# Optimization experiments

Hardware: AMD Instinct MI355X
Metric: run time of the kernel (lower is better)

Reference implementation:

```python
import jax, jax.numpy as jnp
import numpy as np
import math

HEADS = 16
D_MODEL = 1024
HEAD_DIM = D_MODEL // HEADS
B, S = 2, 2048


def setup_inputs() -> dict:
    key = jax.random.key(0)
    ks = jax.random.split(key, 12)
    sc = 1.0 / math.sqrt(D_MODEL)
    inp = {
        "query": jax.random.normal(ks[0], (B, S, D_MODEL), jnp.float32),
        "key_t": jax.random.normal(ks[1], (B, S, D_MODEL), jnp.float32),
        "value": jax.random.normal(ks[2], (B, S, D_MODEL), jnp.float32),
        "mask": jax.random.randint(ks[3], (B, 1, 1, S), 0, 2, jnp.int32),
        "Wq": jax.random.normal(ks[4], (D_MODEL, D_MODEL), jnp.float32) * sc,
        "bq": jnp.zeros((D_MODEL,), jnp.float32),
        "Wk": jax.random.normal(ks[5], (D_MODEL, D_MODEL), jnp.float32) * sc,
        "bk": jnp.zeros((D_MODEL,), jnp.float32),
        "Wv": jax.random.normal(ks[6], (D_MODEL, D_MODEL), jnp.float32) * sc,
        "bv": jnp.zeros((D_MODEL,), jnp.float32),
        "Wo": jax.random.normal(ks[7], (D_MODEL, D_MODEL), jnp.float32) * sc,
        "bo": jnp.zeros((D_MODEL,), jnp.float32),
    }
    return inp


def _split_heads(x):
    # [B, S, D] -> [B, H, S, Dh]
    b, s, _ = x.shape
    return x.reshape(b, s, HEADS, HEAD_DIM).transpose(0, 2, 1, 3)


def reference(query, key_t, value, mask, Wq, bq, Wk, bk, Wv, bv, Wo, bo):
    # Linear projections (torch Linear: x @ W.T + b)
    q = _split_heads(query @ Wq.T + bq)
    k = _split_heads(key_t @ Wk.T + bk)
    v = _split_heads(value @ Wv.T + bv)
    # Scaled dot-product attention; scale by sqrt(head_dim) = query.size(-1) after split
    scores = jnp.einsum("bhqd,bhkd->bhqk", q, k) / math.sqrt(HEAD_DIM)
    scores = jnp.where(mask == 0, jnp.float32(-1e9), scores)
    prob = jax.nn.softmax(scores, axis=-1)
    # dropout is identity at inference
    attn = jnp.einsum("bhqk,bhkd->bhqd", prob, v)
    # [B, H, S, Dh] -> [B, S, D]
    attn = attn.transpose(0, 2, 1, 3).reshape(query.shape[0], -1, D_MODEL)
    return attn @ Wo.T + bo
```

## Files before the change

kernel.cpp:

```cpp
#include <hip/hip_runtime.h>
#include <hip/hip_bf16.h>

typedef __bf16 bf16;
typedef __bf16 bf16x8 __attribute__((ext_vector_type(8)));
typedef __bf16 bf16x4 __attribute__((ext_vector_type(4)));
typedef float  f32x4  __attribute__((ext_vector_type(4)));
typedef float  f32x16 __attribute__((ext_vector_type(16)));

#define AS1 __attribute__((address_space(1)))
#define AS3 __attribute__((address_space(3)))

__device__ __forceinline__ void gload_lds16(const bf16* g, bf16* l) {
    __builtin_amdgcn_global_load_lds((const AS1 unsigned int*)g,
                                     (AS3 unsigned int*)l, 16, 0, 0);
}

__global__ __launch_bounds__(256) void cast8_k(
    const float* __restrict__ s0, const float* __restrict__ s1,
    const float* __restrict__ s2, const float* __restrict__ s3,
    const float* __restrict__ s4, const float* __restrict__ s5,
    const float* __restrict__ s6,
    bf16* __restrict__ d0, bf16* __restrict__ d1, bf16* __restrict__ d2,
    bf16* __restrict__ d3, bf16* __restrict__ d4, bf16* __restrict__ d5,
    bf16* __restrict__ d6,
    const int* __restrict__ m, float* __restrict__ mb,
    int n_big, int n_small) {
    int z = blockIdx.z;
    int i = (blockIdx.x * 256 + threadIdx.x) * 8;
    if (z == 7) {
        if (i >= 4096) return;
        int4 a = *(const int4*)(m + i);
        int4 b = *(const int4*)(m + i + 4);
        float4 o0, o1;
        o0.x = (a.x == 0) ? -1.442695e9f : -17.3123405f;
        o0.y = (a.y == 0) ? -1.442695e9f : -17.3123405f;
        o0.z = (a.z == 0) ? -1.442695e9f : -17.3123405f;
        o0.w = (a.w == 0) ? -1.442695e9f : -17.3123405f;
        o1.x = (b.x == 0) ? -1.442695e9f : -17.3123405f;
        o1.y = (b.y == 0) ? -1.442695e9f : -17.3123405f;
        o1.z = (b.z == 0) ? -1.442695e9f : -17.3123405f;
        o1.w = (b.w == 0) ? -1.442695e9f : -17.3123405f;
        *(float4*)(mb + i) = o0;
        *(float4*)(mb + i + 4) = o1;
        return;
    }
    const float* s = (z == 0) ? s0 : (z == 1) ? s1 : (z == 2) ? s2
                   : (z == 3) ? s3 : (z == 4) ? s4 : (z == 5) ? s5 : s6;
    bf16* d = (z == 0) ? d0 : (z == 1) ? d1 : (z == 2) ? d2
            : (z == 3) ? d3 : (z == 4) ? d4 : (z == 5) ? d5 : d6;
    int n = (z < 3) ? n_big : n_small;
    if (i >= n) return;
    float4 a = *(const float4*)(s + i);
    float4 b = *(const float4*)(s + i + 4);
    bf16x8 o;
    o[0] = (bf16)a.x; o[1] = (bf16)a.y; o[2] = (bf16)a.z; o[3] = (bf16)a.w;
    o[4] = (bf16)b.x; o[5] = (bf16)b.y; o[6] = (bf16)b.z; o[7] = (bf16)b.w;
    *(bf16x8*)(d + i) = o;
}

template <typename OUT_T, bool TRANS>
__device__ __forceinline__ void gemm32_core(
    const bf16* __restrict__ A, const bf16* __restrict__ W,
    const float* __restrict__ bias, OUT_T* __restrict__ C,
    int M, int N, int K) {
    __shared__ bf16 Asm[128 * 64];
    __shared__ bf16 Bsm[128 * 64];
    const int lane = threadIdx.x & 63;
    const int w = threadIdx.x >> 6;
    const int l31 = lane & 31;
    const int h = lane >> 5;
    const int x7 = l31 & 7;
    const int m0 = blockIdx.x * 128;
    const int n0 = blockIdx.y * 128;
    const int srow = lane >> 3;
    const int scol = ((lane & 7) ^ srow) * 8;
    const int wm = (w & 1) * 64;
    const int wn = (w >> 1) * 64;

    f32x16 acc[2][2] = {};

    for (int k0 = 0; k0 < K; k0 += 64) {
#pragma unroll
        for (int c = 0; c < 4; ++c) {
            int r = w * 32 + c * 8;
            gload_lds16(A + (size_t)(m0 + r + srow) * K + k0 + scol, &Asm[r * 64]);
            gload_lds16(W + (size_t)(n0 + r + srow) * K + k0 + scol, &Bsm[r * 64]);
        }
        __syncthreads();
#pragma unroll
        for (int step = 0; step < 4; ++step) {
            bf16x8 af[2], bfv[2];
#pragma unroll
            for (int i = 0; i < 2; ++i)
                af[i] = *(const bf16x8*)&Asm[(wm + i * 32 + l31) * 64 +
                                             (((step * 2 + h) ^ x7) * 8)];
#pragma unroll
            for (int j = 0; j < 2; ++j)
                bfv[j] = *(const bf16x8*)&Bsm[(wn + j * 32 + l31) * 64 +
                                              (((step * 2 + h) ^ x7) * 8)];
#pragma unroll
            for (int i = 0; i < 2; ++i)
#pragma unroll
                for (int j = 0; j < 2; ++j)
                    acc[i][j] = TRANS
                        ? __builtin_amdgcn_mfma_f32_32x32x16_bf16(bfv[j], af[i],
                                                                  acc[i][j], 0, 0, 0)
                        : __builtin_amdgcn_mfma_f32_32x32x16_bf16(af[i], bfv[j],
                                                                  acc[i][j], 0, 0, 0);
        }
        __syncthreads();
    }
    if (!TRANS) {
#pragma unroll
        for (int i = 0; i < 2; ++i)
#pragma unroll
            for (int j = 0; j < 2; ++j) {
                int col = n0 + wn + j * 32 + l31;
                float bv = bias[col];
#pragma unroll
                for (int g = 0; g < 4; ++g)
#pragma unroll
                    for (int rr = 0; rr < 4; ++rr) {
                        int row = m0 + wm + i * 32 + rr + g * 8 + 4 * h;
                        C[(size_t)row * N + col] =
                            (OUT_T)(acc[i][j][g * 4 + rr] + bv);
                    }
            }
    } else {
#pragma unroll
        for (int i = 0; i < 2; ++i) {
            int s = m0 + wm + i * 32 + l31;
            int b = s >> 11;
            int sl = s & 2047;
            int sp = (sl & ~12) | ((sl & 4) << 1) | ((sl & 8) >> 1);
#pragma unroll
            for (int j = 0; j < 2; ++j)
#pragma unroll
                for (int g = 0; g < 4; ++g) {
                    float4 bv4 = *(const float4*)&bias[n0 + wn + j * 32 + g * 8 + 4 * h];
#pragma unroll
                    for (int rr = 0; rr < 4; ++rr) {
                        int n = n0 + wn + j * 32 + g * 8 + 4 * h + rr;
                        C[(size_t)(b * 1024 + n) * 2048 + sp] =
                            (OUT_T)(acc[i][j][g * 4 + rr] + (&bv4.x)[rr]);
                    }
                }
        }
    }
}

__global__ __launch_bounds__(256) void gemm_qkv(
    const bf16* __restrict__ qb, const bf16* __restrict__ kb, const bf16* __restrict__ vb,
    const bf16* __restrict__ Wq, const bf16* __restrict__ Wk, const bf16* __restrict__ Wv,
    const float* __restrict__ bq, const float* __restrict__ bk, const float* __restrict__ bv,
    bf16* __restrict__ Qp, bf16* __restrict__ Kp, bf16* __restrict__ VpT) {
    int z = blockIdx.z;
    if (z == 2) {
        gemm32_core<bf16, true>(vb, Wv, bv, VpT, 4096, 1024, 1024);
    } else {
        const bf16* A = (z == 0) ? qb : kb;
        const bf16* W = (z == 0) ? Wq : Wk;
        const float* bi = (z == 0) ? bq : bk;
        bf16* C = (z == 0) ? Qp : Kp;
        gemm32_core<bf16, false>(A, W, bi, C, 4096, 1024, 1024);
    }
}

__global__ __launch_bounds__(256) void gemm_out_fused(
    const bf16* __restrict__ Op, const float* __restrict__ Lp,
    const bf16* __restrict__ W, const float* __restrict__ bias,
    float* __restrict__ C) {
    __shared__ bf16 Asm[64 * 64];
    __shared__ bf16 Bsm[128 * 64];
    const int id = blockIdx.x;
    const int m0 = (id & 63) * 64;
    const int n0 = (id >> 6) * 128;
    const int lane = threadIdx.x & 63;
    const int w = threadIdx.x >> 6;
    const int l31 = lane & 31;
    const int h = lane >> 5;
    const int x7 = l31 & 7;
    const int srow = lane >> 3;
    const int l7 = lane & 7;
    const int scol = (l7 ^ srow) * 8;
    const int wm = (w & 1) * 32;
    const int wn = (w >> 1) * 64;

    f32x16 acc[2] = {};

    for (int k0 = 0; k0 < 1024; k0 += 64) {
#pragma unroll
        for (int c = 0; c < 2; ++c) {
            int r = w * 16 + c * 8;
            int row = m0 + r + srow;
            int colb = k0 + scol;
            int b = row >> 11, q = row & 2047;
            int hh = colb >> 6, d = colb & 63;
            size_t l0i = (size_t)(b * 16 + hh) * 2048 + q;
            bf16x8 v0 = *(const bf16x8*)&Op[l0i * 64 + d];
            bf16x8 v1 = *(const bf16x8*)&Op[(l0i + 32 * 2048) * 64 + d];
            float inv = 1.0f / (Lp[l0i] + Lp[l0i + 32 * 2048]);
            bf16x8 o;
#pragma unroll
            for (int i = 0; i < 8; ++i)
                o[i] = (bf16)(((float)v0[i] + (float)v1[i]) * inv);
            *(bf16x8*)&Asm[(r + srow) * 64 + l7 * 8] = o;
        }
#pragma unroll
        for (int c = 0; c < 4; ++c) {
            int r = w * 32 + c * 8;
            gload_lds16(W + (size_t)(n0 + r + srow) * 1024 + k0 + scol, &Bsm[r * 64]);
        }
        __syncthreads();
#pragma unroll
        for (int step = 0; step < 4; ++step) {
            bf16x8 af = *(const bf16x8*)&Asm[(wm + l31) * 64 +
                                             (((step * 2 + h) ^ x7) * 8)];
            bf16x8 bfv[2];
#pragma unroll
            for (int j = 0; j < 2; ++j)
                bfv[j] = *(const bf16x8*)&Bsm[(wn + j * 32 + l31) * 64 +
                                              (((step * 2 + h) ^ x7) * 8)];
#pragma unroll
            for (int j = 0; j < 2; ++j)
                acc[j] = __builtin_amdgcn_mfma_f32_32x32x16_bf16(af, bfv[j],
                                                                 acc[j], 0, 0, 0);
        }
        __syncthreads();
    }
#pragma unroll
    for (int j = 0; j < 2; ++j) {
        int col = n0 + wn + j * 32 + l31;
        float bv = bias[col];
#pragma unroll
        for (int g = 0; g < 4; ++g)
#pragma unroll
            for (int rr = 0; rr < 4; ++rr) {
                int row = m0 + wm + rr + g * 8 + 4 * h;
                C[(size_t)row * 1024 + col] = acc[j][g * 4 + rr] + bv;
            }
    }
}

__global__ __launch_bounds__(256, 2) void attn_k(
    const bf16* __restrict__ Qp, const bf16* __restrict__ Kp,
    const bf16* __restrict__ VpT, const float* __restrict__ mb,
    bf16* __restrict__ Opart, float* __restrict__ Lpart) {
    __shared__ bf16 KV[2][2][64 * 64];
    const int g = blockIdx.x;
    const int qb = g >> 6;
    const int bh = (g & 63) >> 1;
    const int sp = g & 1;
    const int b = bh >> 4, hh = bh & 15;
    const int lane = threadIdx.x & 63, w = threadIdx.x >> 6;
    const int l31 = lane & 31, h = lane >> 5;
    const int x7 = l31 & 7;
    const int srow = lane >> 3, scol = ((lane & 7) ^ srow) * 8;
    const float SC = 0.125f * 1.44269504f;
    const int q0 = qb * 256;
    const int k0 = sp * 1024;

    const bf16* Kg = Kp + (size_t)(b * 2048) * 1024 + hh * 64;
    const bf16* Vg = VpT + (size_t)bh * 64 * 2048;
    const float* mbb = mb + b * 2048;

    auto stage = [&](int buf, int kt) {
#pragma unroll
        for (int c = 0; c < 2; ++c) {
            int r = w * 16 + c * 8;
            gload_lds16(Kg + (size_t)(kt + r + srow) * 1024 + scol,
                        &KV[buf][0][r * 64]);
            gload_lds16(Vg + (size_t)(r + srow) * 2048 + kt + scol,
                        &KV[buf][1][r * 64]);
        }
    };
    stage(0, k0);

    bf16x8 qf[2][4];
#pragma unroll
    for (int qg = 0; qg < 2; ++qg) {
        const bf16* Qbase =
            Qp + (size_t)(b * 2048 + q0 + w * 64 + qg * 32 + l31) * 1024 + hh * 64;
#pragma unroll
        for (int step = 0; step < 4; ++step)
            qf[qg][step] = *(const bf16x8*)(Qbase + step * 16 + h * 8);
    }

    f32x16 o[2][2] = {};
    float lsum[2] = {0.0f, 0.0f};

    for (int it = 0; it < 16; ++it) {
        __syncthreads();
        if (it < 15) stage((it + 1) & 1, k0 + (it + 1) * 64);
        const bf16* Ks = KV[it & 1][0];
        const bf16* Vs = KV[it & 1][1];
        const int kt = k0 + it * 64;

        bf16x8 pa[2][4];
#pragma unroll
        for (int kg = 0; kg < 2; ++kg) {
            f32x16 z0 = {}, z1 = {};
#pragma unroll
            for (int step = 0; step < 4; ++step) {
                bf16x8 kf = *(const bf16x8*)&Ks[(kg * 32 + l31) * 64 +
                                                (((step * 2 + h) ^ x7) * 8)];
                z0 = __builtin_amdgcn_mfma_f32_32x32x16_bf16(kf, qf[0][step], z0, 0, 0, 0);
                z1 = __builtin_amdgcn_mfma_f32_32x32x16_bf16(kf, qf[1][step], z1, 0, 0, 0);
            }
#pragma unroll
            for (int g = 0; g < 4; ++g) {
                float4 bia = *(const float4*)&mbb[kt + kg * 32 + g * 8 + 4 * h];
#pragma unroll
                for (int qg = 0; qg < 2; ++qg) {
                    const f32x16& z = qg ? z1 : z0;
                    float p0 = __builtin_amdgcn_exp2f(fmaf(z[g * 4 + 0], SC, bia.x));
                    float p1 = __builtin_amdgcn_exp2f(fmaf(z[g * 4 + 1], SC, bia.y));
                    float p2 = __builtin_amdgcn_exp2f(fmaf(z[g * 4 + 2], SC, bia.z));
                    float p3 = __builtin_amdgcn_exp2f(fmaf(z[g * 4 + 3], SC, bia.w));
                    lsum[qg] += (p0 + p1) + (p2 + p3);
                    bf16x8& pf = pa[qg][kg * 2 + (g >> 1)];
                    int jb = (g & 1) * 4;
                    pf[jb + 0] = (bf16)p0;
                    pf[jb + 1] = (bf16)p1;
                    pf[jb + 2] = (bf16)p2;
                    pf[jb + 3] = (bf16)p3;
                }
            }
        }
#pragma unroll
        for (int t = 0; t < 2; ++t)
#pragma unroll
            for (int kk = 0; kk < 4; ++kk) {
                bf16x8 vf = *(const bf16x8*)&Vs[(t * 32 + l31) * 64 +
                                                (((kk * 2 + h) ^ x7) * 8)];
                o[0][t] = __builtin_amdgcn_mfma_f32_32x32x16_bf16(pa[0][kk], vf, o[0][t], 0, 0, 0);
                o[1][t] = __builtin_amdgcn_mfma_f32_32x32x16_bf16(pa[1][kk], vf, o[1][t], 0, 0, 0);
            }
    }

    const size_t pbase = (size_t)(sp * 32 + bh) * 2048;
#pragma unroll
    for (int qg = 0; qg < 2; ++qg) {
        float ls = lsum[qg] + __shfl_xor(lsum[qg], 32, 64);
        if (h == 0)
            Lpart[pbase + q0 + w * 64 + qg * 32 + l31] = ls;
#pragma unroll
        for (int t = 0; t < 2; ++t)
#pragma unroll
            for (int g = 0; g < 4; ++g)
#pragma unroll
                for (int rr = 0; rr < 4; ++rr) {
                    int q = q0 + w * 64 + qg * 32 + rr + g * 8 + 4 * h;
                    Opart[(pbase + q) * 64 + t * 32 + l31] =
                        (bf16)o[qg][t][g * 4 + rr];
                }
    }
}

extern "C" void kernel_launch(void* const* d_in, const int* in_sizes, int n_in,
                              void* d_out, int out_size, void* d_ws, size_t ws_size,
                              hipStream_t stream) {
    const float* q   = (const float*)d_in[0];
    const float* kt  = (const float*)d_in[1];
    const float* v   = (const float*)d_in[2];
    const int* mask  = (const int*)d_in[3];
    const float* Wq  = (const float*)d_in[4];
    const float* bq  = (const float*)d_in[5];
    const float* Wk  = (const float*)d_in[6];
    const float* bk  = (const float*)d_in[7];
    const float* Wv  = (const float*)d_in[8];
    const float* bv  = (const float*)d_in[9];
    const float* Wo  = (const float*)d_in[10];
    const float* bo  = (const float*)d_in[11];
    float* out = (float*)d_out;

    char* ws = (char*)d_ws;
    const size_t SZ_IN = 4096ull * 1024 * 2;
    const size_t SZ_W  = 1024ull * 1024 * 2;
    bf16* qb  = (bf16*)(ws + 0 * SZ_IN);
    bf16* kb  = (bf16*)(ws + 1 * SZ_IN);
    bf16* vb  = (bf16*)(ws + 2 * SZ_IN);
    bf16* Wqb = (bf16*)(ws + 3 * SZ_IN);
    bf16* Wkb = (bf16*)(ws + 3 * SZ_IN + 1 * SZ_W);
    bf16* Wvb = (bf16*)(ws + 3 * SZ_IN + 2 * SZ_W);
    bf16* Wob = (bf16*)(ws + 3 * SZ_IN + 3 * SZ_W);
    bf16* Qp  = (bf16*)(ws + 3 * SZ_IN + 4 * SZ_W);
    bf16* Kp  = (bf16*)(ws + 4 * SZ_IN + 4 * SZ_W);
    bf16* VpT = (bf16*)(ws + 5 * SZ_IN + 4 * SZ_W);
    float* mb = (float*)(ws + 6 * SZ_IN + 4 * SZ_W);
    char*  p0 = ws + 6 * SZ_IN + 4 * SZ_W + (1 << 20);
    bf16* Opart = (bf16*)p0;
    float* Lpart = (float*)(p0 + 2ull * 32 * 2048 * 64 * 2);

    const int NIN = 4096 * 1024, NW = 1024 * 1024;
    cast8_k<<<dim3(NIN / 2048, 1, 8), 256, 0, stream>>>(
        q, kt, v, Wq, Wk, Wv, Wo, qb, kb, vb, Wqb, Wkb, Wvb, Wob,
        mask, mb, NIN, NW);

    gemm_qkv<<<dim3(32, 8, 3), 256, 0, stream>>>(qb, kb, vb, Wqb, Wkb, Wvb,
                                                 bq, bk, bv, Qp, Kp, VpT);
    attn_k<<<dim3(512), 256, 0, stream>>>(Qp, Kp, VpT, mb, Opart, Lpart);
    gemm_out_fused<<<dim3(512), 256, 0, stream>>>(Opart, Lpart, Wob, bo, out);
}
```

Baseline: 221.2 us.

## Halve attention query tile per block, double grid, add MFMA priority hints

The attention kernel now gives each wave 32 query rows instead of 64, so a block covers 128 queries and the grid grows from 512 to 1024 blocks. Launch bounds rise to 4 blocks per CU, cutting register pressure so more waves can be resident and hide latency. s_setprio hints are added around the MFMA sections so that waves doing matrix work get issue priority over waves running the softmax math. In exchange, each K/V tile staged in LDS is reused by half as many queries, which doubles K/V loads overall.

New measurement: 227.8 us. +3.0%, slower.

```diff
diff --git a/kernel.cpp b/kernel.cpp
--- a/kernel.cpp
+++ b/kernel.cpp
@@ -242,14 +242,14 @@
     }
 }
 
-__global__ __launch_bounds__(256, 2) void attn_k(
+__global__ __launch_bounds__(256, 4) void attn_k(
     const bf16* __restrict__ Qp, const bf16* __restrict__ Kp,
     const bf16* __restrict__ VpT, const float* __restrict__ mb,
     bf16* __restrict__ Opart, float* __restrict__ Lpart) {
     __shared__ bf16 KV[2][2][64 * 64];
     const int g = blockIdx.x;
     const int qb = g >> 6;
-    const int bh = (g & 63) >> 1;
+    const int bh = (g >> 1) & 31;
     const int sp = g & 1;
     const int b = bh >> 4, hh = bh & 15;
     const int lane = threadIdx.x & 63, w = threadIdx.x >> 6;
@@ -257,7 +257,7 @@
     const int x7 = l31 & 7;
     const int srow = lane >> 3, scol = ((lane & 7) ^ srow) * 8;
     const float SC = 0.125f * 1.44269504f;
-    const int q0 = qb * 256;
+    const int q0 = qb * 128;
     const int k0 = sp * 1024;
 
     const bf16* Kg = Kp + (size_t)(b * 2048) * 1024 + hh * 64;
@@ -276,18 +276,17 @@
     };
     stage(0, k0);
 
-    bf16x8 qf[2][4];
-#pragma unroll
-    for (int qg = 0; qg < 2; ++qg) {
+    bf16x8 qf[4];
+    {
         const bf16* Qbase =
-            Qp + (size_t)(b * 2048 + q0 + w * 64 + qg * 32 + l31) * 1024 + hh * 64;
+            Qp + (size_t)(b * 2048 + q0 + w * 32 + l31) * 1024 + hh * 64;
 #pragma unroll
         for (int step = 0; step < 4; ++step)
-            qf[qg][step] = *(const bf16x8*)(Qbase + step * 16 + h * 8);
-    }
-
-    f32x16 o[2][2] = {};
-    float lsum[2] = {0.0f, 0.0f};
+            qf[step] = *(const bf16x8*)(Qbase + step * 16 + h * 8);
+    }
+
+    f32x16 o[2] = {};
+    float lsum = 0.0f;
 
     for (int it = 0; it < 16; ++it) {
         __syncthreads();
@@ -296,65 +295,62 @@
         const bf16* Vs = KV[it & 1][1];
         const int kt = k0 + it * 64;
 
-        bf16x8 pa[2][4];
+        bf16x8 pa[4];
 #pragma unroll
         for (int kg = 0; kg < 2; ++kg) {
-            f32x16 z0 = {}, z1 = {};
+            f32x16 z = {};
+            __builtin_amdgcn_s_setprio(1);
 #pragma unroll
             for (int step = 0; step < 4; ++step) {
                 bf16x8 kf = *(const bf16x8*)&Ks[(kg * 32 + l31) * 64 +
                                                 (((step * 2 + h) ^ x7) * 8)];
-                z0 = __builtin_amdgcn_mfma_f32_32x32x16_bf16(kf, qf[0][step], z0, 0, 0, 0);
-                z1 = __builtin_amdgcn_mfma_f32_32x32x16_bf16(kf, qf[1][step], z1, 0, 0, 0);
-            }
+                z = __builtin_amdgcn_mfma_f32_32x32x16_bf16(kf, qf[step], z, 0, 0, 0);
+            }
+            __builtin_amdgcn_s_setprio(0);
 #pragma unroll
             for (int g = 0; g < 4; ++g) {
                 float4 bia = *(const float4*)&mbb[kt + kg * 32 + g * 8 + 4 * h];
-#pragma unroll
-                for (int qg = 0; qg < 2; ++qg) {
-                    const f32x16& z = qg ? z1 : z0;
-                    float p0 = __builtin_amdgcn_exp2f(fmaf(z[g * 4 + 0], SC, bia.x));
-                    float p1 = __builtin_amdgcn_exp2f(fmaf(z[g * 4 + 1], SC, bia.y));
-                    float p2 = __builtin_amdgcn_exp2f(fmaf(z[g * 4 + 2], SC, bia.z));
-                    float p3 = __builtin_amdgcn_exp2f(fmaf(z[g * 4 + 3], SC, bia.w));
-                    lsum[qg] += (p0 + p1) + (p2 + p3);
-                    bf16x8& pf = pa[qg][kg * 2 + (g >> 1)];
-                    int jb = (g & 1) * 4;
-                    pf[jb + 0] = (bf16)p0;
-                    pf[jb + 1] = (bf16)p1;
-                    pf[jb + 2] = (bf16)p2;
-                    pf[jb + 3] = (bf16)p3;
-                }
-            }
-        }
+                float p0 = __builtin_amdgcn_exp2f(fmaf(z[g * 4 + 0], SC, bia.x));
+                float p1 = __builtin_amdgcn_exp2f(fmaf(z[g * 4 + 1], SC, bia.y));
+                float p2 = __builtin_amdgcn_exp2f(fmaf(z[g * 4 + 2], SC, bia.z));
+                float p3 = __builtin_amdgcn_exp2f(fmaf(z[g * 4 + 3], SC, bia.w));
+                lsum += (p0 + p1) + (p2 + p3);
+                bf16x8& pf = pa[kg * 2 + (g >> 1)];
+                int jb = (g & 1) * 4;
+                pf[jb + 0] = (bf16)p0;
+                pf[jb + 1] = (bf16)p1;
+                pf[jb + 2] = (bf16)p2;
+                pf[jb + 3] = (bf16)p3;
+            }
+        }
+        __builtin_amdgcn_s_setprio(1);
 #pragma unroll
         for (int t = 0; t < 2; ++t)
 #pragma unroll
             for (int kk = 0; kk < 4; ++kk) {
                 bf16x8 vf = *(const bf16x8*)&Vs[(t * 32 + l31) * 64 +
                                                 (((kk * 2 + h) ^ x7) * 8)];
-                o[0][t] = __builtin_amdgcn_mfma_f32_32x32x16_bf16(pa[0][kk], vf, o[0][t], 0, 0, 0);
-                o[1][t] = __builtin_amdgcn_mfma_f32_32x32x16_bf16(pa[1][kk], vf, o[1][t], 0, 0, 0);
-            }
+                o[t] = __builtin_amdgcn_mfma_f32_32x32x16_bf16(pa[kk], vf, o[t], 0, 0, 0);
+            }
+        __builtin_amdgcn_s_setprio(0);
     }
 
     const size_t pbase = (size_t)(sp * 32 + bh) * 2048;
-#pragma unroll
-    for (int qg = 0; qg < 2; ++qg) {
-        float ls = lsum[qg] + __shfl_xor(lsum[qg], 32, 64);
+    {
+        float ls = lsum + __shfl_xor(lsum, 32, 64);
         if (h == 0)
-            Lpart[pbase + q0 + w * 64 + qg * 32 + l31] = ls;
-#pragma unroll
-        for (int t = 0; t < 2; ++t)
-#pragma unroll
-            for (int g = 0; g < 4; ++g)
-#pragma unroll
-                for (int rr = 0; rr < 4; ++rr) {
-                    int q = q0 + w * 64 + qg * 32 + rr + g * 8 + 4 * h;
-                    Opart[(pbase + q) * 64 + t * 32 + l31] =
-                        (bf16)o[qg][t][g * 4 + rr];
-                }
-    }
+            Lpart[pbase + q0 + w * 32 + l31] = ls;
+    }
+#pragma unroll
+    for (int t = 0; t < 2; ++t)
+#pragma unroll
+        for (int g = 0; g < 4; ++g)
+#pragma unroll
+            for (int rr = 0; rr < 4; ++rr) {
+                int q = q0 + w * 32 + rr + g * 8 + 4 * h;
+                Opart[(pbase + q) * 64 + t * 32 + l31] =
+                    (bf16)o[t][g * 4 + rr];
+            }
 }
 
 extern "C" void kernel_launch(void* const* d_in, const int* in_sizes, int n_in,
@@ -399,6 +395,6 @@
 
     gemm_qkv<<<dim3(32, 8, 3), 256, 0, stream>>>(qb, kb, vb, Wqb, Wkb, Wvb,
                                                  bq, bk, bv, Qp, Kp, VpT);
-    attn_k<<<dim3(512), 256, 0, stream>>>(Qp, Kp, VpT, mb, Opart, Lpart);
+    attn_k<<<dim3(1024), 256, 0, stream>>>(Qp, Kp, VpT, mb, Opart, Lpart);
     gemm_out_fused<<<dim3(512), 256, 0, stream>>>(Opart, Lpart, Wob, bo, out);
 }
```

## Fuse fp32-to-bf16 casts into GEMM tile loads and raise MFMA wave priority

Applied to the files above, without the earlier changes.

Removes the separate cast kernel that converted inputs and weights to bf16. The GEMMs now load fp32 directly and convert while staging tiles into LDS, using register loads instead of direct global-to-LDS loads. This drops a full write and read of the bf16 copies, but each GEMM tile reads twice the bytes and loses the async LDS load path. The attention kernel also raises wave priority around its MFMA blocks.

After: 263.9 us. +19.3%, slower.

```diff
diff --git a/kernel.cpp b/kernel.cpp
--- a/kernel.cpp
+++ b/kernel.cpp
@@ -15,52 +15,38 @@
                                      (AS3 unsigned int*)l, 16, 0, 0);
 }
 
-__global__ __launch_bounds__(256) void cast8_k(
-    const float* __restrict__ s0, const float* __restrict__ s1,
-    const float* __restrict__ s2, const float* __restrict__ s3,
-    const float* __restrict__ s4, const float* __restrict__ s5,
-    const float* __restrict__ s6,
-    bf16* __restrict__ d0, bf16* __restrict__ d1, bf16* __restrict__ d2,
-    bf16* __restrict__ d3, bf16* __restrict__ d4, bf16* __restrict__ d5,
-    bf16* __restrict__ d6,
-    const int* __restrict__ m, float* __restrict__ mb,
-    int n_big, int n_small) {
-    int z = blockIdx.z;
+__global__ __launch_bounds__(256) void mask_k(
+    const int* __restrict__ m, float* __restrict__ mb) {
     int i = (blockIdx.x * 256 + threadIdx.x) * 8;
-    if (z == 7) {
-        if (i >= 4096) return;
-        int4 a = *(const int4*)(m + i);
-        int4 b = *(const int4*)(m + i + 4);
-        float4 o0, o1;
-        o0.x = (a.x == 0) ? -1.442695e9f : -17.3123405f;
-        o0.y = (a.y == 0) ? -1.442695e9f : -17.3123405f;
-        o0.z = (a.z == 0) ? -1.442695e9f : -17.3123405f;
-        o0.w = (a.w == 0) ? -1.442695e9f : -17.3123405f;
-        o1.x = (b.x == 0) ? -1.442695e9f : -17.3123405f;
-        o1.y = (b.y == 0) ? -1.442695e9f : -17.3123405f;
-        o1.z = (b.z == 0) ? -1.442695e9f : -17.3123405f;
-        o1.w = (b.w == 0) ? -1.442695e9f : -17.3123405f;
-        *(float4*)(mb + i) = o0;
-        *(float4*)(mb + i + 4) = o1;
-        return;
-    }
-    const float* s = (z == 0) ? s0 : (z == 1) ? s1 : (z == 2) ? s2
-                   : (z == 3) ? s3 : (z == 4) ? s4 : (z == 5) ? s5 : s6;
-    bf16* d = (z == 0) ? d0 : (z == 1) ? d1 : (z == 2) ? d2
-            : (z == 3) ? d3 : (z == 4) ? d4 : (z == 5) ? d5 : d6;
-    int n = (z < 3) ? n_big : n_small;
-    if (i >= n) return;
-    float4 a = *(const float4*)(s + i);
-    float4 b = *(const float4*)(s + i + 4);
+    if (i >= 4096) return;
+    int4 a = *(const int4*)(m + i);
+    int4 b = *(const int4*)(m + i + 4);
+    float4 o0, o1;
+    o0.x = (a.x == 0) ? -1.442695e9f : -17.3123405f;
+    o0.y = (a.y == 0) ? -1.442695e9f : -17.3123405f;
+    o0.z = (a.z == 0) ? -1.442695e9f : -17.3123405f;
+    o0.w = (a.w == 0) ? -1.442695e9f : -17.3123405f;
+    o1.x = (b.x == 0) ? -1.442695e9f : -17.3123405f;
+    o1.y = (b.y == 0) ? -1.442695e9f : -17.3123405f;
+    o1.z = (b.z == 0) ? -1.442695e9f : -17.3123405f;
+    o1.w = (b.w == 0) ? -1.442695e9f : -17.3123405f;
+    *(float4*)(mb + i) = o0;
+    *(float4*)(mb + i + 4) = o1;
+}
+
+__device__ __forceinline__ void stage_f32(const float* __restrict__ src,
+                                          bf16* __restrict__ dst) {
+    float4 a = *(const float4*)src;
+    float4 b = *(const float4*)(src + 4);
     bf16x8 o;
     o[0] = (bf16)a.x; o[1] = (bf16)a.y; o[2] = (bf16)a.z; o[3] = (bf16)a.w;
     o[4] = (bf16)b.x; o[5] = (bf16)b.y; o[6] = (bf16)b.z; o[7] = (bf16)b.w;
-    *(bf16x8*)(d + i) = o;
+    *(bf16x8*)dst = o;
 }
 
 template <typename OUT_T, bool TRANS>
 __device__ __forceinline__ void gemm32_core(
-    const bf16* __restrict__ A, const bf16* __restrict__ W,
+    const float* __restrict__ A, const float* __restrict__ W,
     const float* __restrict__ bias, OUT_T* __restrict__ C,
     int M, int N, int K) {
     __shared__ bf16 Asm[128 * 64];
@@ -83,8 +69,10 @@
 #pragma unroll
         for (int c = 0; c < 4; ++c) {
             int r = w * 32 + c * 8;
-            gload_lds16(A + (size_t)(m0 + r + srow) * K + k0 + scol, &Asm[r * 64]);
-            gload_lds16(W + (size_t)(n0 + r + srow) * K + k0 + scol, &Bsm[r * 64]);
+            stage_f32(A + (size_t)(m0 + r + srow) * K + k0 + scol,
+                      &Asm[r * 64 + lane * 8]);
+            stage_f32(W + (size_t)(n0 + r + srow) * K + k0 + scol,
+                      &Bsm[r * 64 + lane * 8]);
         }
         __syncthreads();
 #pragma unroll
@@ -150,16 +138,16 @@
 }
 
 __global__ __launch_bounds__(256) void gemm_qkv(
-    const bf16* __restrict__ qb, const bf16* __restrict__ kb, const bf16* __restrict__ vb,
-    const bf16* __restrict__ Wq, const bf16* __restrict__ Wk, const bf16* __restrict__ Wv,
+    const float* __restrict__ qf, const float* __restrict__ ktf, const float* __restrict__ vf,
+    const float* __restrict__ Wq, const float* __restrict__ Wk, const float* __restrict__ Wv,
     const float* __restrict__ bq, const float* __restrict__ bk, const float* __restrict__ bv,
     bf16* __restrict__ Qp, bf16* __restrict__ Kp, bf16* __restrict__ VpT) {
     int z = blockIdx.z;
     if (z == 2) {
-        gemm32_core<bf16, true>(vb, Wv, bv, VpT, 4096, 1024, 1024);
+        gemm32_core<bf16, true>(vf, Wv, bv, VpT, 4096, 1024, 1024);
     } else {
-        const bf16* A = (z == 0) ? qb : kb;
-        const bf16* W = (z == 0) ? Wq : Wk;
+        const float* A = (z == 0) ? qf : ktf;
+        const float* W = (z == 0) ? Wq : Wk;
         const float* bi = (z == 0) ? bq : bk;
         bf16* C = (z == 0) ? Qp : Kp;
         gemm32_core<bf16, false>(A, W, bi, C, 4096, 1024, 1024);
@@ -168,7 +156,7 @@
 
 __global__ __launch_bounds__(256) void gemm_out_fused(
     const bf16* __restrict__ Op, const float* __restrict__ Lp,
-    const bf16* __restrict__ W, const float* __restrict__ bias,
+    const float* __restrict__ W, const float* __restrict__ bias,
     float* __restrict__ C) {
     __shared__ bf16 Asm[64 * 64];
     __shared__ bf16 Bsm[128 * 64];
@@ -209,7 +197,8 @@
 #pragma unroll
         for (int c = 0; c < 4; ++c) {
             int r = w * 32 + c * 8;
-            gload_lds16(W + (size_t)(n0 + r + srow) * 1024 + k0 + scol, &Bsm[r * 64]);
+            stage_f32(W + (size_t)(n0 + r + srow) * 1024 + k0 + scol,
+                      &Bsm[r * 64 + lane * 8]);
         }
         __syncthreads();
 #pragma unroll
@@ -300,6 +289,7 @@
 #pragma unroll
         for (int kg = 0; kg < 2; ++kg) {
             f32x16 z0 = {}, z1 = {};
+            __builtin_amdgcn_s_setprio(1);
 #pragma unroll
             for (int step = 0; step < 4; ++step) {
                 bf16x8 kf = *(const bf16x8*)&Ks[(kg * 32 + l31) * 64 +
@@ -307,6 +297,7 @@
                 z0 = __builtin_amdgcn_mfma_f32_32x32x16_bf16(kf, qf[0][step], z0, 0, 0, 0);
                 z1 = __builtin_amdgcn_mfma_f32_32x32x16_bf16(kf, qf[1][step], z1, 0, 0, 0);
             }
+            __builtin_amdgcn_s_setprio(0);
 #pragma unroll
             for (int g = 0; g < 4; ++g) {
                 float4 bia = *(const float4*)&mbb[kt + kg * 32 + g * 8 + 4 * h];
@@ -327,6 +318,7 @@
                 }
             }
         }
+        __builtin_amdgcn_s_setprio(1);
 #pragma unroll
         for (int t = 0; t < 2; ++t)
 #pragma unroll
@@ -336,6 +328,7 @@
                 o[0][t] = __builtin_amdgcn_mfma_f32_32x32x16_bf16(pa[0][kk], vf, o[0][t], 0, 0, 0);
                 o[1][t] = __builtin_amdgcn_mfma_f32_32x32x16_bf16(pa[1][kk], vf, o[1][t], 0, 0, 0);
             }
+        __builtin_amdgcn_s_setprio(0);
     }
 
     const size_t pbase = (size_t)(sp * 32 + bh) * 2048;
@@ -376,29 +369,18 @@
 
     char* ws = (char*)d_ws;
     const size_t SZ_IN = 4096ull * 1024 * 2;
-    const size_t SZ_W  = 1024ull * 1024 * 2;
-    bf16* qb  = (bf16*)(ws + 0 * SZ_IN);
-    bf16* kb  = (bf16*)(ws + 1 * SZ_IN);
-    bf16* vb  = (bf16*)(ws + 2 * SZ_IN);
-    bf16* Wqb = (bf16*)(ws + 3 * SZ_IN);
-    bf16* Wkb = (bf16*)(ws + 3 * SZ_IN + 1 * SZ_W);
-    bf16* Wvb = (bf16*)(ws + 3 * SZ_IN + 2 * SZ_W);
-    bf16* Wob = (bf16*)(ws + 3 * SZ_IN + 3 * SZ_W);
-    bf16* Qp  = (bf16*)(ws + 3 * SZ_IN + 4 * SZ_W);
-    bf16* Kp  = (bf16*)(ws + 4 * SZ_IN + 4 * SZ_W);
-    bf16* VpT = (bf16*)(ws + 5 * SZ_IN + 4 * SZ_W);
-    float* mb = (float*)(ws + 6 * SZ_IN + 4 * SZ_W);
-    char*  p0 = ws + 6 * SZ_IN + 4 * SZ_W + (1 << 20);
+    bf16* Qp  = (bf16*)(ws + 0 * SZ_IN);
+    bf16* Kp  = (bf16*)(ws + 1 * SZ_IN);
+    bf16* VpT = (bf16*)(ws + 2 * SZ_IN);
+    float* mb = (float*)(ws + 3 * SZ_IN);
+    char*  p0 = ws + 3 * SZ_IN + (1 << 20);
     bf16* Opart = (bf16*)p0;
     float* Lpart = (float*)(p0 + 2ull * 32 * 2048 * 64 * 2);
 
-    const int NIN = 4096 * 1024, NW = 1024 * 1024;
-    cast8_k<<<dim3(NIN / 2048, 1, 8), 256, 0, stream>>>(
-        q, kt, v, Wq, Wk, Wv, Wo, qb, kb, vb, Wqb, Wkb, Wvb, Wob,
-        mask, mb, NIN, NW);
-
-    gemm_qkv<<<dim3(32, 8, 3), 256, 0, stream>>>(qb, kb, vb, Wqb, Wkb, Wvb,
+    mask_k<<<dim3(2), 256, 0, stream>>>(mask, mb);
+
+    gemm_qkv<<<dim3(32, 8, 3), 256, 0, stream>>>(q, kt, v, Wq, Wk, Wv,
                                                  bq, bk, bv, Qp, Kp, VpT);
     attn_k<<<dim3(512), 256, 0, stream>>>(Qp, Kp, VpT, mb, Opart, Lpart);
-    gemm_out_fused<<<dim3(512), 256, 0, stream>>>(Opart, Lpart, Wob, bo, out);
-}
+    gemm_out_fused<<<dim3(512), 256, 0, stream>>>(Opart, Lpart, Wo, bo, out);
+}
```
